# Kernel optimization log

Measured on AMD Instinct MI355X. Metric: run time of the kernel, lower is better.

The kernel has to match this reference:

```python
import jax, jax.numpy as jnp
import numpy as np

EMBED_DIM = 2048
NUM_EXPERTS = 16  # num_local_experts + 1 shared global expert
TOP_K = 2


def setup_inputs() -> dict:
    key = jax.random.key(0)
    kx, kw = jax.random.split(key)
    x = jax.random.normal(kx, (8, 4096, EMBED_DIM), dtype=jnp.float32)
    # nn.Linear(embed_dim, total_experts, bias=False) weight: [num_experts, embed_dim]
    bound = 1.0 / np.sqrt(EMBED_DIM)
    gate_w = jax.random.uniform(kw, (NUM_EXPERTS, EMBED_DIM), dtype=jnp.float32,
                                minval=-bound, maxval=bound)
    return {"x": x, "gate_w": gate_w}


def reference(x, gate_w):
    # logits: [B, L, E]
    logits = jnp.einsum("bld,ed->ble", x, gate_w)
    probs = jax.nn.softmax(logits, axis=-1)
    weights, indices = jax.lax.top_k(probs, TOP_K)  # [B, L, K] each
    weights = weights / jnp.sum(weights, axis=-1, keepdims=True)
    return weights, indices
```

## Files before the change

kernel.cpp:

```cpp
#include <hip/hip_runtime.h>
#include <cstdint>

#define EMBED      2048
#define NEXP       16
#define NWAVES     8
#define TOKB       64
#define WINF       64
#define NWIN       (EMBED / WINF)
#define NBUF       4
#define NTOK_TOTAL (8 * 4096)
#define WOFF       (NTOK_TOTAL * 2)
#define PAD        17

__device__ __forceinline__ void g2l16(const float* g, float* l) {
    __builtin_amdgcn_global_load_lds(
        (const __attribute__((address_space(1))) void*)(uintptr_t)g,
        (__attribute__((address_space(3))) void*)(uintptr_t)l,
        16, 0, 0);
}
__device__ __forceinline__ void g2l4(const float* g, float* l) {
    __builtin_amdgcn_global_load_lds(
        (const __attribute__((address_space(1))) void*)(uintptr_t)g,
        (__attribute__((address_space(3))) void*)(uintptr_t)l,
        4, 0, 0);
}

extern "C" __global__ __launch_bounds__(NWAVES * 64, 4)
void router_kernel(const float* __restrict__ x,
                   const float* __restrict__ gw,
                   float* __restrict__ out)
{
    __shared__ float lds_x[NBUF][TOKB * WINF];
    __shared__ float lds_w[NBUF][NEXP * WINF];

    const int tid  = threadIdx.x;
    const int lane = tid & 63;
    const int W    = __builtin_amdgcn_readfirstlane(tid >> 6);
    const int t0   = blockIdx.x * TOKB;

    float acc[NEXP];
#pragma unroll
    for (int e = 0; e < NEXP; ++e) acc[e] = 0.0f;

    auto stage_x = [&](int win, int buf) {
#pragma unroll
        for (int it = 0; it < 2; ++it) {
            const int G    = it * 512 + tid;
            const int row  = G >> 4;
            const int pos  = G & 15;
            const int gsrc = (pos & 8) | ((pos ^ row) & 7);
            const float* src = x + (size_t)(t0 + row) * EMBED + win * WINF + gsrc * 4;
            g2l16(src, &lds_x[buf][G * 4]);
        }
    };

    auto stage_w = [&](int win, int buf) {
#pragma unroll
        for (int it = 0; it < 2; ++it) {
            const int q = it * 512 + tid;
            const int e = q >> 6;
            const int f = q & 63;
            g2l4(gw + e * EMBED + win * WINF + f, &lds_w[buf][q]);
        }
    };

    auto compute = [&](int win, int buf) {
        const float* bx = lds_x[buf];
        const float* bw = lds_w[buf];
#pragma unroll
        for (int j = 0; j < 2; ++j) {
            const int g   = W * 2 + j;
            const int pos = (g & 8) | ((g ^ lane) & 7);
            const float4 x4 = *(const float4*)&bx[lane * WINF + pos * 4];
#pragma unroll
            for (int e = 0; e < NEXP; ++e) {
                const float4 w4 = *(const float4*)&bw[e * WINF + g * 4];
                acc[e] = fmaf(x4.x, w4.x, acc[e]);
                acc[e] = fmaf(x4.y, w4.y, acc[e]);
                acc[e] = fmaf(x4.z, w4.z, acc[e]);
                acc[e] = fmaf(x4.w, w4.w, acc[e]);
            }
        }
    };

    stage_x(0, 0); stage_w(0, 0);
    stage_x(1, 1); stage_w(1, 1);
    stage_x(2, 2); stage_w(2, 2);
    asm volatile("s_waitcnt vmcnt(8)" ::: "memory");
    __builtin_amdgcn_s_barrier();
    asm volatile("" ::: "memory");

    for (int win = 0; win < NWIN - 3; ++win) {
        stage_x(win + 3, (win + 3) & 3);
        stage_w(win + 3, (win + 3) & 3);
        compute(win, win & 3);
        asm volatile("s_waitcnt vmcnt(8) lgkmcnt(0)" ::: "memory");
        __builtin_amdgcn_s_barrier();
        asm volatile("" ::: "memory");
    }
    compute(NWIN - 3, (NWIN - 3) & 3);
    asm volatile("s_waitcnt vmcnt(4) lgkmcnt(0)" ::: "memory");
    __builtin_amdgcn_s_barrier();
    asm volatile("" ::: "memory");
    compute(NWIN - 2, (NWIN - 2) & 3);
    asm volatile("s_waitcnt vmcnt(0) lgkmcnt(0)" ::: "memory");
    __builtin_amdgcn_s_barrier();
    asm volatile("" ::: "memory");
    compute(NWIN - 1, (NWIN - 1) & 3);

    float (*part)[TOKB][PAD] = (float (*)[TOKB][PAD])lds_x;
#pragma unroll
    for (int e = 0; e < NEXP; ++e) part[W][lane][e] = acc[e];
    __syncthreads();

    if (tid < TOKB) {
        float tot[NEXP];
#pragma unroll
        for (int e = 0; e < NEXP; ++e) tot[e] = 0.0f;
#pragma unroll
        for (int w = 0; w < NWAVES; ++w) {
#pragma unroll
            for (int e = 0; e < NEXP; ++e) tot[e] += part[w][tid][e];
        }

        float m1 = tot[0]; int i1 = 0;
#pragma unroll
        for (int e = 1; e < NEXP; ++e) {
            if (tot[e] > m1) { m1 = tot[e]; i1 = e; }
        }
        float m2 = -INFINITY; int i2 = 0;
#pragma unroll
        for (int e = 0; e < NEXP; ++e) {
            const bool sel = (e != i1) && (tot[e] > m2);
            if (sel) { m2 = tot[e]; i2 = e; }
        }

        const float ed = __expf(m2 - m1);
        const float w1 = 1.0f / (1.0f + ed);
        const float w2 = 1.0f - w1;

        const int t = t0 + tid;
        out[t * 2 + 0] = w1;
        out[t * 2 + 1] = w2;
        out[WOFF + t * 2 + 0] = (float)i1;
        out[WOFF + t * 2 + 1] = (float)i2;
    }
}

extern "C" void kernel_launch(void* const* d_in, const int* in_sizes, int n_in,
                              void* d_out, int out_size, void* d_ws, size_t ws_size,
                              hipStream_t stream) {
    const float* x  = (const float*)d_in[0];
    const float* gw = (const float*)d_in[1];
    float* out = (float*)d_out;

    const int nblocks = NTOK_TOTAL / TOKB;
    router_kernel<<<dim3(nblocks), dim3(NWAVES * 64), 0, stream>>>(x, gw, out);
}
```

Baseline: 64.66 us.

## Double tokens per block to reuse gate weight loads across two token rows

Raises tokens per block from 64 to 128, so each lane accumulates two tokens and every gate-weight float4 read from LDS is reused twice. The x swizzle becomes a full 4-bit XOR and the pipeline loop is restructured to wait and barrier before issuing the next stage, with an added sync before the partial-sum reuse of LDS. The aim is fewer weight LDS reads and less per-block overhead. In exchange it doubles LDS use and register pressure, lowers the occupancy hint to 2, and halves the number of blocks.

Result: slower. 71.10 us (+10.0%).

```diff
diff --git a/kernel.cpp b/kernel.cpp
--- a/kernel.cpp
+++ b/kernel.cpp
@@ -4,7 +4,7 @@
 #define EMBED      2048
 #define NEXP       16
 #define NWAVES     8
-#define TOKB       64
+#define TOKB       128
 #define WINF       64
 #define NWIN       (EMBED / WINF)
 #define NBUF       4
@@ -15,17 +15,15 @@
 __device__ __forceinline__ void g2l16(const float* g, float* l) {
     __builtin_amdgcn_global_load_lds(
         (const __attribute__((address_space(1))) void*)(uintptr_t)g,
-        (__attribute__((address_space(3))) void*)(uintptr_t)l,
-        16, 0, 0);
+        (__attribute__((address_space(3))) void*)(uintptr_t)l, 16, 0, 0);
 }
 __device__ __forceinline__ void g2l4(const float* g, float* l) {
     __builtin_amdgcn_global_load_lds(
         (const __attribute__((address_space(1))) void*)(uintptr_t)g,
-        (__attribute__((address_space(3))) void*)(uintptr_t)l,
-        4, 0, 0);
+        (__attribute__((address_space(3))) void*)(uintptr_t)l, 4, 0, 0);
 }
 
-extern "C" __global__ __launch_bounds__(NWAVES * 64, 4)
+extern "C" __global__ __launch_bounds__(NWAVES * 64, 2)
 void router_kernel(const float* __restrict__ x,
                    const float* __restrict__ gw,
                    float* __restrict__ out)
@@ -38,79 +36,78 @@
     const int W    = __builtin_amdgcn_readfirstlane(tid >> 6);
     const int t0   = blockIdx.x * TOKB;
 
-    float acc[NEXP];
+    float acc0[NEXP], acc1[NEXP];
 #pragma unroll
-    for (int e = 0; e < NEXP; ++e) acc[e] = 0.0f;
+    for (int e = 0; e < NEXP; ++e) { acc0[e] = 0.0f; acc1[e] = 0.0f; }
 
-    auto stage_x = [&](int win, int buf) {
+    auto stage = [&](int win, int buf) {
 #pragma unroll
-        for (int it = 0; it < 2; ++it) {
-            const int G    = it * 512 + tid;
-            const int row  = G >> 4;
-            const int pos  = G & 15;
-            const int gsrc = (pos & 8) | ((pos ^ row) & 7);
-            const float* src = x + (size_t)(t0 + row) * EMBED + win * WINF + gsrc * 4;
-            g2l16(src, &lds_x[buf][G * 4]);
+        for (int it = 0; it < 4; ++it) {
+            const int L    = it * 512 + tid;
+            const int row  = L >> 4;
+            const int slot = L & 15;
+            const int gsrc = slot ^ (row & 15);
+            g2l16(x + (size_t)(t0 + row) * EMBED + win * WINF + gsrc * 4,
+                  &lds_x[buf][L * 4]);
         }
-    };
-
-    auto stage_w = [&](int win, int buf) {
 #pragma unroll
         for (int it = 0; it < 2; ++it) {
             const int q = it * 512 + tid;
-            const int e = q >> 6;
-            const int f = q & 63;
+            const int e = q >> 6, f = q & 63;
             g2l4(gw + e * EMBED + win * WINF + f, &lds_w[buf][q]);
         }
     };
 
-    auto compute = [&](int win, int buf) {
+    auto compute = [&](int buf) {
         const float* bx = lds_x[buf];
         const float* bw = lds_w[buf];
 #pragma unroll
         for (int j = 0; j < 2; ++j) {
-            const int g   = W * 2 + j;
-            const int pos = (g & 8) | ((g ^ lane) & 7);
-            const float4 x4 = *(const float4*)&bx[lane * WINF + pos * 4];
+            const int g    = W * 2 + j;
+            const int slot = (g ^ lane) & 15;
+            const float4 xa = *(const float4*)&bx[lane * WINF + slot * 4];
+            const float4 xb = *(const float4*)&bx[(lane + 64) * WINF + slot * 4];
 #pragma unroll
             for (int e = 0; e < NEXP; ++e) {
                 const float4 w4 = *(const float4*)&bw[e * WINF + g * 4];
-                acc[e] = fmaf(x4.x, w4.x, acc[e]);
-                acc[e] = fmaf(x4.y, w4.y, acc[e]);
-                acc[e] = fmaf(x4.z, w4.z, acc[e]);
-                acc[e] = fmaf(x4.w, w4.w, acc[e]);
+                acc0[e] = fmaf(xa.x, w4.x, acc0[e]);
+                acc0[e] = fmaf(xa.y, w4.y, acc0[e]);
+                acc0[e] = fmaf(xa.z, w4.z, acc0[e]);
+                acc0[e] = fmaf(xa.w, w4.w, acc0[e]);
+                acc1[e] = fmaf(xb.x, w4.x, acc1[e]);
+                acc1[e] = fmaf(xb.y, w4.y, acc1[e]);
+                acc1[e] = fmaf(xb.z, w4.z, acc1[e]);
+                acc1[e] = fmaf(xb.w, w4.w, acc1[e]);
             }
         }
     };
 
-    stage_x(0, 0); stage_w(0, 0);
-    stage_x(1, 1); stage_w(1, 1);
-    stage_x(2, 2); stage_w(2, 2);
-    asm volatile("s_waitcnt vmcnt(8)" ::: "memory");
+    stage(0, 0); stage(1, 1); stage(2, 2);
+
+    for (int k = 0; k <= NWIN - 3; ++k) {
+        asm volatile("s_waitcnt vmcnt(12) lgkmcnt(0)" ::: "memory");
+        __builtin_amdgcn_s_barrier();
+        asm volatile("" ::: "memory");
+        if (k + 3 < NWIN) stage(k + 3, (k + 3) & 3);
+        compute(k & 3);
+    }
+    asm volatile("s_waitcnt vmcnt(6) lgkmcnt(0)" ::: "memory");
     __builtin_amdgcn_s_barrier();
     asm volatile("" ::: "memory");
-
-    for (int win = 0; win < NWIN - 3; ++win) {
-        stage_x(win + 3, (win + 3) & 3);
-        stage_w(win + 3, (win + 3) & 3);
-        compute(win, win & 3);
-        asm volatile("s_waitcnt vmcnt(8) lgkmcnt(0)" ::: "memory");
-        __builtin_amdgcn_s_barrier();
-        asm volatile("" ::: "memory");
-    }
-    compute(NWIN - 3, (NWIN - 3) & 3);
-    asm volatile("s_waitcnt vmcnt(4) lgkmcnt(0)" ::: "memory");
-    __builtin_amdgcn_s_barrier();
-    asm volatile("" ::: "memory");
-    compute(NWIN - 2, (NWIN - 2) & 3);
+    compute((NWIN - 2) & 3);
     asm volatile("s_waitcnt vmcnt(0) lgkmcnt(0)" ::: "memory");
     __builtin_amdgcn_s_barrier();
     asm volatile("" ::: "memory");
-    compute(NWIN - 1, (NWIN - 1) & 3);
+    compute((NWIN - 1) & 3);
+
+    __syncthreads();
 
     float (*part)[TOKB][PAD] = (float (*)[TOKB][PAD])lds_x;
 #pragma unroll
-    for (int e = 0; e < NEXP; ++e) part[W][lane][e] = acc[e];
+    for (int e = 0; e < NEXP; ++e) {
+        part[W][lane][e]      = acc0[e];
+        part[W][lane + 64][e] = acc1[e];
+    }
     __syncthreads();
 
     if (tid < TOKB) {
```
